# Kernel tuning notes

Measured on AMD Instinct MI355X. Metric: run time of the kernel, lower is better.

## Reference

```python
import jax, jax.numpy as jnp
import numpy as np

B, SEQ, DIM = 1, 2048, 4096
N_HEADS, N_KV, HEAD_DIM = 32, 8, 128
N_REP = N_HEADS // N_KV
MAX_CTX = 4096


def setup_inputs() -> dict:
    key = jax.random.key(0)
    ks = jax.random.split(key, 6)
    x = jax.random.normal(ks[0], (B, SEQ, DIM), jnp.float32)
    # RoPE table: (1, SEQ, 1, HEAD_DIM//2, 2) with [cos, sin] in last dim
    inv_freq = 1.0 / (10000.0 ** (jnp.arange(0, HEAD_DIM, 2, dtype=jnp.float32) / HEAD_DIM))
    t = jnp.arange(SEQ, dtype=jnp.float32)
    ang = t[:, None] * inv_freq[None, :]
    freqs_cis = jnp.stack([jnp.cos(ang), jnp.sin(ang)], axis=-1).reshape(1, SEQ, 1, HEAD_DIM // 2, 2)
    cache_kv = jnp.zeros((2, 1, MAX_CTX, N_KV, HEAD_DIM), jnp.float32)
    s = 0.02
    wq = jax.random.normal(ks[1], (DIM, N_HEADS * HEAD_DIM), jnp.float32) * s
    wk = jax.random.normal(ks[2], (DIM, N_KV * HEAD_DIM), jnp.float32) * s
    wv = jax.random.normal(ks[3], (DIM, N_KV * HEAD_DIM), jnp.float32) * s
    wo = jax.random.normal(ks[4], (N_HEADS * HEAD_DIM, DIM), jnp.float32) * s
    return {"x": x, "cache_kv": cache_kv, "freqs_cis": freqs_cis,
            "wq": wq, "wk": wk, "wv": wv, "wo": wo, "start_pos": 0}


def _rope(t, freqs_cis):
    # t: (b, s, h, head_dim); freqs_cis: (1, s, 1, head_dim//2, 2)
    tr = t.reshape(*t.shape[:-1], -1, 2)
    a, b = tr[..., 0], tr[..., 1]
    c, d = freqs_cis[..., 0], freqs_cis[..., 1]
    return jnp.stack([a * c - b * d, a * d + b * c], axis=-1).reshape(t.shape)


def reference(x, cache_kv, freqs_cis, wq, wk, wv, wo, start_pos):
    b, s, _ = x.shape
    xq = (x @ wq).reshape(b, s, N_HEADS, HEAD_DIM)
    xk = (x @ wk).reshape(b, s, N_KV, HEAD_DIM)
    xv = (x @ wv).reshape(b, s, N_KV, HEAD_DIM)
    xq = _rope(xq, freqs_cis)
    xk = _rope(xk, freqs_cis)
    # KV-cache scatter write (start_pos is a static Python int)
    cache = cache_kv.at[:, :, start_pos:start_pos + s].set(jnp.stack([xk, xv]))
    L = start_pos + s
    keys = cache[0, :, :L]    # (b, L, kv, hd)
    values = cache[1, :, :L]
    # GQA without materializing repeats: group q heads by kv head
    q = xq.transpose(0, 2, 1, 3).reshape(b, N_KV, N_REP, s, HEAD_DIM)
    k = keys.transpose(0, 2, 1, 3)     # (b, kv, L, hd)
    v = values.transpose(0, 2, 1, 3)
    scores = jnp.einsum('bkrqd,bkld->bkrql', q, k) * (HEAD_DIM ** -0.5)
    if s > 1:
        mask = jnp.triu(jnp.full((s, L), -jnp.inf, jnp.float32), k=start_pos + 1)
        scores = scores + mask
    p = jax.nn.softmax(scores, axis=-1)
    out = jnp.einsum('bkrql,bkld->bkrqd', p, v)          # (b, kv, rep, s, hd)
    out = out.reshape(b, N_HEADS, s, HEAD_DIM).transpose(0, 2, 1, 3).reshape(b, s, N_HEADS * HEAD_DIM)
    return out @ wo
```

## Files before the change

### kernel.cpp

```cpp
#include <hip/hip_runtime.h>
#include <hip/hip_bf16.h>
#include <stdint.h>

#define SEQ   2048
#define DIM   4096
#define NH    32
#define NKV   8
#define HD    128
#define NREP  4
#define QKVN  6144
#define KOFF  4096
#define VOFF  5120

typedef __bf16 bf16;
typedef __attribute__((ext_vector_type(8))) __bf16 bf16x8;
typedef __attribute__((ext_vector_type(4))) __bf16 bf16x4;
typedef __attribute__((ext_vector_type(4))) float  f32x4;
typedef __attribute__((address_space(1))) void as1_void;
typedef __attribute__((address_space(3))) void as3_void;

__device__ __forceinline__ void async_copy16(void* lds, const void* g) {
  __builtin_amdgcn_global_load_lds((as1_void*)(void*)g, (as3_void*)lds, 16, 0, 0);
}

__device__ __forceinline__ uint32_t pack2bf(float a, float b) {
  union { bf16 h; uint16_t u; } ca, cb;
  ca.h = (bf16)a; cb.h = (bf16)b;
  return (uint32_t)ca.u | ((uint32_t)cb.u << 16);
}

__global__ __launch_bounds__(256) void cast_x_kernel(const float* __restrict__ src,
                                                     bf16* __restrict__ dst) {
  size_t i = ((size_t)blockIdx.x * 256 + threadIdx.x) * 4;
  const float4 v = *(const float4*)(src + i);
  bf16x4 o;
  o[0] = (bf16)v.x; o[1] = (bf16)v.y; o[2] = (bf16)v.z; o[3] = (bf16)v.w;
  *(bf16x4*)(dst + i) = o;
}

__global__ __launch_bounds__(256) void transpose_cast_kernel(const float* __restrict__ src,
                                                             bf16* __restrict__ dst,
                                                             int R, int C) {
  __shared__ float tile[64][65];
  const int c0 = blockIdx.x * 64, r0 = blockIdx.y * 64;
  const int tx = threadIdx.x & 15, ty = threadIdx.x >> 4;
#pragma unroll
  for (int p = 0; p < 4; ++p) {
    float4 v = *(const float4*)&src[(size_t)(r0 + ty + p*16) * C + c0 + tx*4];
    tile[ty + p*16][tx*4+0] = v.x;
    tile[ty + p*16][tx*4+1] = v.y;
    tile[ty + p*16][tx*4+2] = v.z;
    tile[ty + p*16][tx*4+3] = v.w;
  }
  __syncthreads();
  const int k = threadIdx.x & 15;
  const int g = threadIdx.x >> 4;
#pragma unroll
  for (int p = 0; p < 4; ++p) {
    int X = g + 16*p;
    bf16x4 o;
    o[0] = (bf16)tile[4*k+0][X];
    o[1] = (bf16)tile[4*k+1][X];
    o[2] = (bf16)tile[4*k+2][X];
    o[3] = (bf16)tile[4*k+3][X];
    *(bf16x4*)&dst[(size_t)(c0 + X) * R + r0 + 4*k] = o;
  }
}

template<int OUT_F32, int ROPE>
__global__ __launch_bounds__(256) void gemm_bt_kernel(const bf16* __restrict__ A,
                                                      const bf16* __restrict__ Bt,
                                                      void* __restrict__ Cout,
                                                      int M, int N, int K,
                                                      const float* __restrict__ fr) {
  __shared__ __align__(16) bf16 As[2*128*32];
  __shared__ __align__(16) bf16 Bs[2*128*32];
  const int tid = threadIdx.x;
  const int w = tid >> 6, lane = tid & 63;
  const int lane16 = lane & 15, quad = lane >> 4;
  const int wr = w >> 1, wc = w & 1;
  const int bm = blockIdx.y * 128, bn = blockIdx.x * 128;
  const bf16* a0 = A  + (size_t)bm * K;
  const bf16* b0 = Bt + (size_t)bn * K;
  f32x4 acc[4][4] = {};
  for (int k0 = 0; k0 < K; k0 += 64) {
    __syncthreads();
#pragma unroll
    for (int i = 0; i < 4; ++i) {
      int c = tid + i * 256;
      int kk = c >> 9, rem = c & 511;
      async_copy16(&As[c*8], a0 + (size_t)(rem >> 2) * K + k0 + kk*32 + (rem & 3) * 8);
      async_copy16(&Bs[c*8], b0 + (size_t)(rem >> 2) * K + k0 + kk*32 + (rem & 3) * 8);
    }
    __syncthreads();
#pragma unroll
    for (int kk = 0; kk < 2; ++kk) {
      bf16x8 af[4];
#pragma unroll
      for (int i = 0; i < 4; ++i)
        af[i] = *(const bf16x8*)&As[kk*4096 + (wr*64 + i*16 + lane16)*32 + quad*8];
#pragma unroll
      for (int j = 0; j < 4; ++j) {
        bf16x8 bfrag = *(const bf16x8*)&Bs[kk*4096 + (wc*64 + j*16 + lane16)*32 + quad*8];
#pragma unroll
        for (int i = 0; i < 4; ++i)
          acc[i][j] = __builtin_amdgcn_mfma_f32_16x16x32_bf16(af[i], bfrag, acc[i][j], 0, 0, 0);
      }
    }
  }
#pragma unroll
  for (int i = 0; i < 4; ++i)
#pragma unroll
    for (int j = 0; j < 4; ++j) {
      const bool do_rope = ROPE && (bn + wc*64 + j*16) < 5120;
      const int p2 = (bn + wc*64 + j*16 + lane16) & 126;
#pragma unroll
      for (int r = 0; r < 4; ++r) {
        size_t row = (size_t)bm + wr*64 + i*16 + quad*4 + r;
        size_t col = (size_t)bn + wc*64 + j*16 + lane16;
        float v = acc[i][j][r];
        if (ROPE) {
          float vp = __shfl_xor(v, 1);
          if (do_rope) {
            float2 cd = *(const float2*)&fr[row*128 + p2];
            v = (lane16 & 1) ? (vp*cd.y + v*cd.x) : (v*cd.x - vp*cd.y);
          }
        }
        if (OUT_F32) ((float*)Cout)[row * N + col] = v;
        else         ((bf16*)Cout)[row * N + col] = (bf16)v;
      }
    }
}

__global__ __launch_bounds__(256) void transpose_v_kernel(const bf16* __restrict__ qkv,
                                                          bf16* __restrict__ vt) {
  __shared__ bf16 tile[32][33];
  int tt = blockIdx.x * 32;
  int dd = blockIdx.y * 32;
  int kv = blockIdx.z;
  int tx = threadIdx.x & 31, ty = threadIdx.x >> 5;
  const bf16* src = qkv + VOFF + kv * HD;
#pragma unroll
  for (int j = 0; j < 4; ++j)
    tile[ty + j*8][tx] = src[(size_t)(tt + ty + j*8) * QKVN + dd + tx];
  __syncthreads();
  bf16* dst = vt + ((size_t)kv * HD + dd) * SEQ + tt;
#pragma unroll
  for (int j = 0; j < 4; ++j)
    dst[(size_t)(ty + j*8) * SEQ + tx] = tile[tx][ty + j*8];
}

__global__ __launch_bounds__(256, 3) void flash_attn_kernel(const bf16* __restrict__ qkv,
                                                            const bf16* __restrict__ vt,
                                                            bf16* __restrict__ out) {
  __shared__ __align__(16) bf16 Ks[4*96*32];
  __shared__ __align__(16) bf16 Vts[3*128*32];
  const int b  = blockIdx.x;
  const int qt = 31 - (b >> 5);
  const int h  = b & 31;
  const int kvh = h >> 2;
  const int tid = threadIdx.x;
  const int w = tid >> 6, lane = tid & 63;
  const int lane16 = lane & 15, quad = lane >> 4;
  const float scale = 0.08838834764831845f;
  const int qglob = qt*64 + w*16 + lane16;

  const bf16* qrow = qkv + (size_t)qglob * QKVN + h * HD + quad*8;
  bf16x8 qreg[4];
#pragma unroll
  for (int kk = 0; kk < 4; ++kk)
    qreg[kk] = *(const bf16x8*)(qrow + kk*32);

  f32x4 acc_o[8] = {};
  float m_s = -3e38f, l_s = 0.f;

  const bf16* kbase0 = qkv + KOFF + kvh * HD;
  const bf16* vbase0 = vt + (size_t)kvh * HD * SEQ;

  const int L = (qt*64 + 159) / 96;
  for (int jj = 0; jj < L; ++jj) {
    const int kv0 = jj * 96;
    __syncthreads();
#pragma unroll
    for (int i = 0; i < 6; ++i) {
      int c = tid + i * 256;
      {
        int kk = c / 384, rem = c - kk*384;
        async_copy16(&Ks[c*8], kbase0 + (size_t)(kv0 + (rem >> 2)) * QKVN + kk*32 + (rem & 3) * 8);
      }
      {
        int kk2 = c >> 9, cp = c & 511;
        async_copy16(&Vts[c*8], vbase0 + (size_t)(cp >> 2) * SEQ + kv0 + kk2*32 + (cp & 3) * 8);
      }
    }
    __syncthreads();

    f32x4 accT[6] = {};
#pragma unroll
    for (int kk = 0; kk < 4; ++kk)
#pragma unroll
      for (int jn = 0; jn < 6; ++jn) {
        bf16x8 kf = *(const bf16x8*)&Ks[(kk*96 + jn*16 + lane16)*32 + quad*8];
        accT[jn] = __builtin_amdgcn_mfma_f32_16x16x32_bf16(kf, qreg[kk], accT[jn], 0, 0, 0);
      }

    float s[6][4];
#pragma unroll
    for (int jn = 0; jn < 6; ++jn)
#pragma unroll
      for (int r = 0; r < 4; ++r) {
        float v = accT[jn][r] * scale;
        if ((kv0 + jn*16 + quad*4 + r) > qglob) v = -3e38f;
        s[jn][r] = v;
      }

    float mt = s[0][0];
#pragma unroll
    for (int jn = 0; jn < 6; ++jn)
#pragma unroll
      for (int r = 0; r < 4; ++r) mt = fmaxf(mt, s[jn][r]);
    mt = fmaxf(mt, __shfl_xor(mt, 16));
    mt = fmaxf(mt, __shfl_xor(mt, 32));
    float mnew = fmaxf(m_s, mt);
    float alpha = __expf(m_s - mnew);
    m_s = mnew;
    float rs = 0.f;
#pragma unroll
    for (int jn = 0; jn < 6; ++jn)
#pragma unroll
      for (int r = 0; r < 4; ++r) {
        float p = __expf(s[jn][r] - mnew);
        s[jn][r] = p;
        rs += p;
      }
    rs += __shfl_xor(rs, 16);
    rs += __shfl_xor(rs, 32);
    l_s = l_s * alpha + rs;

    float alpha_row[4];
#pragma unroll
    for (int r = 0; r < 4; ++r)
      alpha_row[r] = __shfl(alpha, quad*4 + r);
#pragma unroll
    for (int jd = 0; jd < 8; ++jd)
#pragma unroll
      for (int r = 0; r < 4; ++r) acc_o[jd][r] *= alpha_row[r];

    uint32_t pk[6][2];
#pragma unroll
    for (int jn = 0; jn < 6; ++jn) {
      pk[jn][0] = pack2bf(s[jn][0], s[jn][1]);
      pk[jn][1] = pack2bf(s[jn][2], s[jn][3]);
    }

    const int src0 = (quad & 1) * 32 + lane16;
    const int src1 = src0 + 16;
    const bool hi = quad >= 2;
#pragma unroll
    for (int kk2 = 0; kk2 < 3; ++kk2) {
      uint32_t v0l = __shfl(pk[2*kk2][0],   src0), v0h = __shfl(pk[2*kk2][1],   src0);
      uint32_t v1l = __shfl(pk[2*kk2][0],   src1), v1h = __shfl(pk[2*kk2][1],   src1);
      uint32_t w0l = __shfl(pk[2*kk2+1][0], src0), w0h = __shfl(pk[2*kk2+1][1], src0);
      uint32_t w1l = __shfl(pk[2*kk2+1][0], src1), w1h = __shfl(pk[2*kk2+1][1], src1);
      union { uint32_t u[4]; bf16x8 v; } af;
      af.u[0] = hi ? w0l : v0l;
      af.u[1] = hi ? w0h : v0h;
      af.u[2] = hi ? w1l : v1l;
      af.u[3] = hi ? w1h : v1h;
#pragma unroll
      for (int jd = 0; jd < 8; ++jd) {
        bf16x8 vf = *(const bf16x8*)&Vts[(kk2*128 + jd*16 + lane16)*32 + quad*8];
        acc_o[jd] = __builtin_amdgcn_mfma_f32_16x16x32_bf16(af.v, vf, acc_o[jd], 0, 0, 0);
      }
    }
  }

  const float inv_l = 1.f / l_s;
  float linv[4];
#pragma unroll
  for (int r = 0; r < 4; ++r)
    linv[r] = __shfl(inv_l, quad*4 + r);

  bf16* obase = out + (size_t)(qt*64 + w*16) * DIM + h * HD;
#pragma unroll
  for (int jd = 0; jd < 8; ++jd)
#pragma unroll
    for (int r = 0; r < 4; ++r)
      obase[(size_t)(quad*4 + r) * DIM + jd*16 + lane16] = (bf16)(acc_o[jd][r] * linv[r]);
}

extern "C" void kernel_launch(void* const* d_in, const int* in_sizes, int n_in,
                              void* d_out, int out_size, void* d_ws, size_t ws_size,
                              hipStream_t stream) {
  const float* x  = (const float*)d_in[0];
  const float* fr = (const float*)d_in[2];
  const float* wq = (const float*)d_in[3];
  const float* wk = (const float*)d_in[4];
  const float* wv = (const float*)d_in[5];
  const float* wo = (const float*)d_in[6];
  float* out = (float*)d_out;

  char* ws = (char*)d_ws;
  bf16* xb     = (bf16*)(ws);
  bf16* wqkv_t = (bf16*)(ws + 16777216);
  bf16* wo_t   = (bf16*)(ws + 67108864);
  bf16* qkv    = (bf16*)(ws + 100663296);
  bf16* vt     = (bf16*)(ws + 125829120);
  bf16* attn   = (bf16*)(ws + 130023424);
  (void)ws_size; (void)in_sizes; (void)n_in; (void)out_size;

  cast_x_kernel<<<8192, 256, 0, stream>>>(x, xb);
  transpose_cast_kernel<<<dim3(64,64), 256, 0, stream>>>(wq, wqkv_t, DIM, DIM);
  transpose_cast_kernel<<<dim3(16,64), 256, 0, stream>>>(wk, wqkv_t + (size_t)4096*4096, DIM, 1024);
  transpose_cast_kernel<<<dim3(16,64), 256, 0, stream>>>(wv, wqkv_t + (size_t)5120*4096, DIM, 1024);
  transpose_cast_kernel<<<dim3(64,64), 256, 0, stream>>>(wo, wo_t, DIM, DIM);

  gemm_bt_kernel<0,1><<<dim3(48,16), 256, 0, stream>>>(xb, wqkv_t, qkv, SEQ, QKVN, DIM, fr);
  transpose_v_kernel<<<dim3(64,4,8), 256, 0, stream>>>(qkv, vt);
  flash_attn_kernel<<<1024, 256, 0, stream>>>(qkv, vt, attn);
  gemm_bt_kernel<1,0><<<dim3(32,16), 256, 0, stream>>>(attn, wo_t, out, SEQ, DIM, DIM, nullptr);
}
```

Before: 532.8 us.

## Replace GEMM with 256x256 tile, 8-wave, double-buffered swizzled pipeline

Rewrites the projection GEMMs to use 256x256 tiles with 512 threads, double-buffered LDS with async global-to-LDS copies interleaved between MFMA phases, an XOR-swizzled LDS layout, workgroup ID remapping and s_setprio around MFMA blocks. The goal is to hide global load latency behind compute and raise per-block data reuse. In exchange it uses 128KB of LDS per block and far fewer blocks (192 and 128) on a GPU with many CUs, which can leave CUs idle and cause tail imbalance.

```diff
diff --git a/kernel.cpp b/kernel.cpp
--- a/kernel.cpp
+++ b/kernel.cpp
@@ -27,6 +27,12 @@
   union { bf16 h; uint16_t u; } ca, cb;
   ca.h = (bf16)a; cb.h = (bf16)b;
   return (uint32_t)ca.u | ((uint32_t)cb.u << 16);
+}
+
+__device__ __forceinline__ void block_barrier() {
+  asm volatile("" ::: "memory");
+  __builtin_amdgcn_s_barrier();
+  asm volatile("" ::: "memory");
 }
 
 __global__ __launch_bounds__(256) void cast_x_kernel(const float* __restrict__ src,
@@ -68,56 +74,131 @@
 }
 
 template<int OUT_F32, int ROPE>
-__global__ __launch_bounds__(256) void gemm_bt_kernel(const bf16* __restrict__ A,
-                                                      const bf16* __restrict__ Bt,
-                                                      void* __restrict__ Cout,
-                                                      int M, int N, int K,
-                                                      const float* __restrict__ fr) {
-  __shared__ __align__(16) bf16 As[2*128*32];
-  __shared__ __align__(16) bf16 Bs[2*128*32];
-  const int tid = threadIdx.x;
-  const int w = tid >> 6, lane = tid & 63;
+__global__ __launch_bounds__(512, 2) void gemm256_kernel(const bf16* __restrict__ A,
+                                                         const bf16* __restrict__ Bt,
+                                                         void* __restrict__ Cout,
+                                                         int M, int N, int K,
+                                                         const float* __restrict__ fr) {
+  __shared__ __align__(16) bf16 As[32768];
+  __shared__ __align__(16) bf16 Bs[32768];
+  char* AsB = (char*)As;
+  char* BsB = (char*)Bs;
+
+  const int tid  = threadIdx.x;
+  const int w    = tid >> 6, lane = tid & 63;
   const int lane16 = lane & 15, quad = lane >> 4;
-  const int wr = w >> 1, wc = w & 1;
-  const int bm = blockIdx.y * 128, bn = blockIdx.x * 128;
-  const bf16* a0 = A  + (size_t)bm * K;
-  const bf16* b0 = Bt + (size_t)bn * K;
-  f32x4 acc[4][4] = {};
-  for (int k0 = 0; k0 < K; k0 += 64) {
-    __syncthreads();
-#pragma unroll
-    for (int i = 0; i < 4; ++i) {
-      int c = tid + i * 256;
-      int kk = c >> 9, rem = c & 511;
-      async_copy16(&As[c*8], a0 + (size_t)(rem >> 2) * K + k0 + kk*32 + (rem & 3) * 8);
-      async_copy16(&Bs[c*8], b0 + (size_t)(rem >> 2) * K + k0 + kk*32 + (rem & 3) * 8);
-    }
-    __syncthreads();
-#pragma unroll
-    for (int kk = 0; kk < 2; ++kk) {
-      bf16x8 af[4];
-#pragma unroll
-      for (int i = 0; i < 4; ++i)
-        af[i] = *(const bf16x8*)&As[kk*4096 + (wr*64 + i*16 + lane16)*32 + quad*8];
-#pragma unroll
-      for (int j = 0; j < 4; ++j) {
-        bf16x8 bfrag = *(const bf16x8*)&Bs[kk*4096 + (wc*64 + j*16 + lane16)*32 + quad*8];
-#pragma unroll
-        for (int i = 0; i < 4; ++i)
-          acc[i][j] = __builtin_amdgcn_mfma_f32_16x16x32_bf16(af[i], bfrag, acc[i][j], 0, 0, 0);
-      }
-    }
+  const int wm = w >> 2, wn = w & 3;
+
+  const int nwg = gridDim.x * gridDim.y;
+  int bid = blockIdx.y * gridDim.x + blockIdx.x;
+  bid = (bid & 7) * (nwg >> 3) + (bid >> 3);
+  const int bx = bid % gridDim.x, by = bid / gridDim.x;
+  const int bm = by * 256, bn = bx * 256;
+
+  const int NT = K >> 6;
+
+  const int qsw = ((quad ^ (lane16 & 3)) << 4);
+  const uint32_t aLane = (uint32_t)(wm*128 + lane16) * 64 + qsw;
+  const uint32_t bLane = (uint32_t)(wn*64  + lane16) * 64 + qsw;
+
+  auto stageA = [&](int buf, int t, int ks) {
+#pragma unroll
+    for (int i = 0; i < 2; ++i) {
+      int c = tid + (i << 9);
+      int row = c >> 2;
+      int q = ((c & 3) ^ (row & 3)) << 3;
+      async_copy16(AsB + buf*32768 + ks*16384 + c*16,
+                   A + (size_t)(bm + row) * K + t*64 + ks*32 + q);
+    }
+  };
+  auto stageB = [&](int buf, int t, int ks) {
+#pragma unroll
+    for (int i = 0; i < 2; ++i) {
+      int c = tid + (i << 9);
+      int row = c >> 2;
+      int q = ((c & 3) ^ (row & 3)) << 3;
+      async_copy16(BsB + buf*32768 + ks*16384 + c*16,
+                   Bt + (size_t)(bn + row) * K + t*64 + ks*32 + q);
+    }
+  };
+
+  f32x4 acc[8][4] = {};
+
+#define LD_A(DST, BUF, KS, QM)                                                        \
+  do {                                                                                \
+    _Pragma("unroll")                                                                 \
+    for (int ii = 0; ii < 4; ++ii)                                                    \
+      (DST)[ii] = *(const bf16x8*)(AsB + (BUF)*32768 + (KS)*16384 + aLane             \
+                                   + ((QM)*4 + ii) * 1024);                           \
+  } while (0)
+#define LD_B(DST, BUF, KS)                                                            \
+  do {                                                                                \
+    _Pragma("unroll")                                                                 \
+    for (int jj = 0; jj < 4; ++jj)                                                    \
+      (DST)[jj] = *(const bf16x8*)(BsB + (BUF)*32768 + (KS)*16384 + bLane             \
+                                   + jj * 1024);                                      \
+  } while (0)
+#define MMA_PHASE(AF, BF, QM)                                                         \
+  do {                                                                                \
+    __builtin_amdgcn_s_setprio(1);                                                    \
+    _Pragma("unroll")                                                                 \
+    for (int jj = 0; jj < 4; ++jj)                                                    \
+      _Pragma("unroll")                                                               \
+      for (int ii = 0; ii < 4; ++ii)                                                  \
+        acc[(QM)*4 + ii][jj] = __builtin_amdgcn_mfma_f32_16x16x32_bf16(               \
+            (AF)[ii], (BF)[jj], acc[(QM)*4 + ii][jj], 0, 0, 0);                       \
+    __builtin_amdgcn_s_setprio(0);                                                    \
+  } while (0)
+
+  stageA(0, 0, 0); stageB(0, 0, 0); stageA(0, 0, 1); stageB(0, 0, 1);
+  stageA(1, 1, 0); stageB(1, 1, 0);
+  asm volatile("s_waitcnt vmcnt(4)" ::: "memory");
+  block_barrier();
+
+  for (int t = 0; t < NT; ++t) {
+    const int cb = t & 1, nb = cb ^ 1;
+    bf16x8 af[4], bf0[4], bf1[4];
+
+    LD_A(af, cb, 0, 0);
+    LD_B(bf0, cb, 0);
+    if (t + 1 < NT) stageA(nb, t + 1, 1);
+    block_barrier();
+    MMA_PHASE(af, bf0, 0);
+    block_barrier();
+
+    LD_A(af, cb, 0, 1);
+    if (t + 1 < NT) stageB(nb, t + 1, 1);
+    block_barrier();
+    MMA_PHASE(af, bf0, 1);
+    block_barrier();
+
+    LD_A(af, cb, 1, 0);
+    LD_B(bf1, cb, 1);
+    if (t + 2 < NT) stageA(cb, t + 2, 0);
+    block_barrier();
+    MMA_PHASE(af, bf1, 0);
+    block_barrier();
+
+    LD_A(af, cb, 1, 1);
+    if (t + 2 < NT) stageB(cb, t + 2, 0);
+    block_barrier();
+    MMA_PHASE(af, bf1, 1);
+    if (t + 2 < NT) asm volatile("s_waitcnt vmcnt(4)" ::: "memory");
+    else            asm volatile("s_waitcnt vmcnt(0)" ::: "memory");
+    block_barrier();
   }
-#pragma unroll
-  for (int i = 0; i < 4; ++i)
+
+#pragma unroll
+  for (int i = 0; i < 8; ++i)
 #pragma unroll
     for (int j = 0; j < 4; ++j) {
-      const bool do_rope = ROPE && (bn + wc*64 + j*16) < 5120;
-      const int p2 = (bn + wc*64 + j*16 + lane16) & 126;
+      const int colb = bn + wn*64 + j*16;
+      const bool do_rope = ROPE && colb < 5120;
+      const int p2 = (colb + lane16) & 126;
 #pragma unroll
       for (int r = 0; r < 4; ++r) {
-        size_t row = (size_t)bm + wr*64 + i*16 + quad*4 + r;
-        size_t col = (size_t)bn + wc*64 + j*16 + lane16;
+        size_t row = (size_t)bm + wm*128 + i*16 + quad*4 + r;
+        size_t col = (size_t)colb + lane16;
         float v = acc[i][j][r];
         if (ROPE) {
           float vp = __shfl_xor(v, 1);
@@ -130,6 +211,9 @@
         else         ((bf16*)Cout)[row * N + col] = (bf16)v;
       }
     }
+#undef LD_A
+#undef LD_B
+#undef MMA_PHASE
 }
 
 __global__ __launch_bounds__(256) void transpose_v_kernel(const bf16* __restrict__ qkv,
@@ -315,8 +399,8 @@
   transpose_cast_kernel<<<dim3(16,64), 256, 0, stream>>>(wv, wqkv_t + (size_t)5120*4096, DIM, 1024);
   transpose_cast_kernel<<<dim3(64,64), 256, 0, stream>>>(wo, wo_t, DIM, DIM);
 
-  gemm_bt_kernel<0,1><<<dim3(48,16), 256, 0, stream>>>(xb, wqkv_t, qkv, SEQ, QKVN, DIM, fr);
+  gemm256_kernel<0,1><<<dim3(24,8), 512, 0, stream>>>(xb, wqkv_t, qkv, SEQ, QKVN, DIM, fr);
   transpose_v_kernel<<<dim3(64,4,8), 256, 0, stream>>>(qkv, vt);
   flash_attn_kernel<<<1024, 256, 0, stream>>>(qkv, vt, attn);
-  gemm_bt_kernel<1,0><<<dim3(32,16), 256, 0, stream>>>(attn, wo_t, out, SEQ, DIM, DIM, nullptr);
-}
+  gemm256_kernel<1,0><<<dim3(16,8), 512, 0, stream>>>(attn, wo_t, out, SEQ, DIM, DIM, nullptr);
+}
```

Result: slower. 625.6 us (+17.4%).

## Swizzle GEMM LDS layout, shrink N tiles, and remap block ids across XCDs

Applied to the files above, without the earlier changes.

Replaces the GEMM kernel with a version that stages 64-wide K slabs in LDS using an XOR swizzle on 16-byte chunks. The goal is to remove bank conflicts on the fragment reads. The N tile becomes a template parameter: 96 for the QKV projection and 64 for the output projection, which launches 1024 workgroups each instead of 768 or 512. A block-id remap strides consecutive workgroups across the 8 XCDs. Smaller N tiles cut data reuse per block and add more A-tile reloads, in exchange for more parallelism and better cache locality per XCD.

```diff
diff --git a/kernel.cpp b/kernel.cpp
--- a/kernel.cpp
+++ b/kernel.cpp
@@ -67,57 +67,81 @@
   }
 }
 
-template<int OUT_F32, int ROPE>
-__global__ __launch_bounds__(256) void gemm_bt_kernel(const bf16* __restrict__ A,
-                                                      const bf16* __restrict__ Bt,
-                                                      void* __restrict__ Cout,
-                                                      int M, int N, int K,
-                                                      const float* __restrict__ fr) {
-  __shared__ __align__(16) bf16 As[2*128*32];
-  __shared__ __align__(16) bf16 Bs[2*128*32];
-  const int tid = threadIdx.x;
-  const int w = tid >> 6, lane = tid & 63;
+template<int OUT_F32, int ROPE, int BN>
+__global__ __launch_bounds__(256) void gemm_bt2_kernel(const bf16* __restrict__ A,
+                                                       const bf16* __restrict__ Bt,
+                                                       void* __restrict__ Cout,
+                                                       int M, int N, int K,
+                                                       const float* __restrict__ fr) {
+  constexpr int BNF = BN / 32;
+  __shared__ __align__(16) char ldsA[128 * 128];
+  __shared__ __align__(16) char ldsB[BN * 128];
+
+  const int tid  = threadIdx.x;
+  const int w    = tid >> 6, lane = tid & 63;
   const int lane16 = lane & 15, quad = lane >> 4;
   const int wr = w >> 1, wc = w & 1;
-  const int bm = blockIdx.y * 128, bn = blockIdx.x * 128;
-  const bf16* a0 = A  + (size_t)bm * K;
-  const bf16* b0 = Bt + (size_t)bn * K;
-  f32x4 acc[4][4] = {};
+
+  const int nwg = gridDim.x * gridDim.y;
+  int bid = blockIdx.y * gridDim.x + blockIdx.x;
+  bid = (bid & 7) * (nwg >> 3) + (bid >> 3);
+  const int bx = bid % gridDim.x, by = bid / gridDim.x;
+  const int bm = by * 128, bn = bx * BN;
+
+  f32x4 acc[4][BNF] = {};
+
   for (int k0 = 0; k0 < K; k0 += 64) {
     __syncthreads();
 #pragma unroll
     for (int i = 0; i < 4; ++i) {
-      int c = tid + i * 256;
-      int kk = c >> 9, rem = c & 511;
-      async_copy16(&As[c*8], a0 + (size_t)(rem >> 2) * K + k0 + kk*32 + (rem & 3) * 8);
-      async_copy16(&Bs[c*8], b0 + (size_t)(rem >> 2) * K + k0 + kk*32 + (rem & 3) * 8);
+      int c = tid + (i << 8);
+      int row = c >> 3, sl = c & 7;
+      async_copy16(ldsA + c*16,
+                   A + (size_t)(bm + row) * K + k0 + ((sl ^ (row & 7)) << 3));
+    }
+#pragma unroll
+    for (int i = 0; i < BNF; ++i) {
+      int c = tid + (i << 8);
+      int col = c >> 3, sl = c & 7;
+      async_copy16(ldsB + c*16,
+                   Bt + (size_t)(bn + col) * K + k0 + ((sl ^ (col & 7)) << 3));
     }
     __syncthreads();
 #pragma unroll
-    for (int kk = 0; kk < 2; ++kk) {
-      bf16x8 af[4];
-#pragma unroll
-      for (int i = 0; i < 4; ++i)
-        af[i] = *(const bf16x8*)&As[kk*4096 + (wr*64 + i*16 + lane16)*32 + quad*8];
-#pragma unroll
-      for (int j = 0; j < 4; ++j) {
-        bf16x8 bfrag = *(const bf16x8*)&Bs[kk*4096 + (wc*64 + j*16 + lane16)*32 + quad*8];
-#pragma unroll
-        for (int i = 0; i < 4; ++i)
-          acc[i][j] = __builtin_amdgcn_mfma_f32_16x16x32_bf16(af[i], bfrag, acc[i][j], 0, 0, 0);
-      }
+    for (int ks = 0; ks < 2; ++ks) {
+      bf16x8 af[4], bfg[BNF];
+#pragma unroll
+      for (int ii = 0; ii < 4; ++ii) {
+        int row_ = wr*64 + ii*16 + lane16;
+        int S_ = (ks*4 + quad) ^ (lane16 & 7);
+        af[ii] = *(const bf16x8*)(ldsA + row_*128 + S_*16);
+      }
+#pragma unroll
+      for (int jj = 0; jj < BNF; ++jj) {
+        int col_ = wc*(BN/2) + jj*16 + lane16;
+        int S_ = (ks*4 + quad) ^ (lane16 & 7);
+        bfg[jj] = *(const bf16x8*)(ldsB + col_*128 + S_*16);
+      }
+#pragma unroll
+      for (int jj = 0; jj < BNF; ++jj)
+#pragma unroll
+        for (int ii = 0; ii < 4; ++ii)
+          acc[ii][jj] = __builtin_amdgcn_mfma_f32_16x16x32_bf16(af[ii], bfg[jj],
+                                                                acc[ii][jj], 0, 0, 0);
     }
   }
+
 #pragma unroll
   for (int i = 0; i < 4; ++i)
 #pragma unroll
-    for (int j = 0; j < 4; ++j) {
-      const bool do_rope = ROPE && (bn + wc*64 + j*16) < 5120;
-      const int p2 = (bn + wc*64 + j*16 + lane16) & 126;
+    for (int j = 0; j < BNF; ++j) {
+      const int colb = bn + wc*(BN/2) + j*16;
+      const bool do_rope = ROPE && colb < 5120;
+      const int p2 = (colb + lane16) & 126;
 #pragma unroll
       for (int r = 0; r < 4; ++r) {
         size_t row = (size_t)bm + wr*64 + i*16 + quad*4 + r;
-        size_t col = (size_t)bn + wc*64 + j*16 + lane16;
+        size_t col = (size_t)colb + lane16;
         float v = acc[i][j][r];
         if (ROPE) {
           float vp = __shfl_xor(v, 1);
@@ -315,8 +339,8 @@
   transpose_cast_kernel<<<dim3(16,64), 256, 0, stream>>>(wv, wqkv_t + (size_t)5120*4096, DIM, 1024);
   transpose_cast_kernel<<<dim3(64,64), 256, 0, stream>>>(wo, wo_t, DIM, DIM);
 
-  gemm_bt_kernel<0,1><<<dim3(48,16), 256, 0, stream>>>(xb, wqkv_t, qkv, SEQ, QKVN, DIM, fr);
+  gemm_bt2_kernel<0,1,96><<<dim3(64,16), 256, 0, stream>>>(xb, wqkv_t, qkv, SEQ, QKVN, DIM, fr);
   transpose_v_kernel<<<dim3(64,4,8), 256, 0, stream>>>(qkv, vt);
   flash_attn_kernel<<<1024, 256, 0, stream>>>(qkv, vt, attn);
-  gemm_bt_kernel<1,0><<<dim3(32,16), 256, 0, stream>>>(attn, wo_t, out, SEQ, DIM, DIM, nullptr);
-}
+  gemm_bt2_kernel<1,0,64><<<dim3(64,16), 256, 0, stream>>>(attn, wo_t, out, SEQ, DIM, DIM, nullptr);
+}
```

Result: slower. 588.5 us (+10.5%).
